# Optimization experiments

Measured on AMD Instinct MI355X. Metric: run time of the kernel, lower is better.

## Reference

```python
import jax, jax.numpy as jnp
import numpy as np


def setup_inputs() -> dict:
    key = jax.random.key(0)
    k1, k2 = jax.random.split(key)
    N = 4_194_304
    n, m = 63, 64
    x = jax.random.uniform(k1, (N,), dtype=jnp.float32)
    coefficients = jax.random.normal(k2, (n + 1 + m,), dtype=jnp.float32)
    return {"x": x, "coefficients": coefficients, "n": n, "m": m}


def reference(x, coefficients, n, m):
    # Split coefficients: numerator uses powers x^0..x^n, denominator x^1..x^m.
    n_coeffs = coefficients[: n + 1]
    m_coeffs = coefficients[n + 1 :]
    # x_powers_num: (n+1, N); tiny vector-matmul reduces power axis.
    exps_num = jnp.arange(n + 1, dtype=x.dtype)[:, None]
    numerator = jnp.einsum("p,pn->n", n_coeffs, x[None, :] ** exps_num)
    exps_den = jnp.arange(1, m + 1, dtype=x.dtype)[:, None]
    denominator = jnp.einsum("p,pn->n", m_coeffs, x[None, :] ** exps_den)
    return numerator / (jnp.abs(denominator) + 1.0)
```

## Files before the change

kernel.cpp:

```cpp
#include <hip/hip_runtime.h>


typedef float v2f __attribute__((ext_vector_type(2)));

#define EPT 8

__global__ __launch_bounds__(256) void rationals_kernel(
    const float* __restrict__ x,
    const float* __restrict__ coeff,
    float* __restrict__ out, int N) {
    int idx = (blockIdx.x * blockDim.x + threadIdx.x) * EPT;
    if (idx >= N) return;

    float xs[EPT];
    float4 xa = *reinterpret_cast<const float4*>(x + idx);
    float4 xb = *reinterpret_cast<const float4*>(x + idx + 4);
    xs[0] = xa.x; xs[1] = xa.y; xs[2] = xa.z; xs[3] = xa.w;
    xs[4] = xb.x; xs[5] = xb.y; xs[6] = xb.z; xs[7] = xb.w;

    v2f xx[EPT], h[EPT];
    float cn_top = coeff[63];
    float cd_top = coeff[127];
#pragma unroll
    for (int j = 0; j < EPT; ++j) {
        xx[j] = (v2f){xs[j], xs[j]};
        h[j]  = (v2f){cn_top, cd_top};
    }

#pragma unroll
    for (int p = 62; p >= 0; --p) {
        v2f c2 = {coeff[p], coeff[64 + p]};
#pragma unroll
        for (int j = 0; j < EPT; ++j)
            h[j] = __builtin_elementwise_fma(h[j], xx[j], c2);
    }

    float o[EPT];
#pragma unroll
    for (int j = 0; j < EPT; ++j) {
        float den = h[j].y * xs[j];
        o[j] = h[j].x * __builtin_amdgcn_rcpf(fabsf(den) + 1.0f);
    }
    *reinterpret_cast<float4*>(out + idx)     = (float4){o[0], o[1], o[2], o[3]};
    *reinterpret_cast<float4*>(out + idx + 4) = (float4){o[4], o[5], o[6], o[7]};
}

extern "C" void kernel_launch(void* const* d_in, const int* in_sizes, int n_in,
                              void* d_out, int out_size, void* d_ws, size_t ws_size,
                              hipStream_t stream) {
    const float* x     = (const float*)d_in[0];
    const float* coeff = (const float*)d_in[1];
    float* out = (float*)d_out;
    int N = in_sizes[0];

    int threads = 256;
    int elems_per_block = threads * EPT;
    int blocks = (N + elems_per_block - 1) / elems_per_block;
    rationals_kernel<<<blocks, threads, 0, stream>>>(x, coeff, out, N);
}
```

Before: 16.96 us.

## Split packed num/den Horner into separate scalar loops with 16 elements per thread

Replaces the paired v2f FMA, which evaluated numerator and denominator together, with two separate scalar Horner loops. Elements per thread rise from 8 to 16 to add independent FMA chains. This risks losing packed-FMA throughput unless the compiler re-packs adjacent elements, and it raises register pressure.

```diff
diff --git a/kernel.cpp b/kernel.cpp
--- a/kernel.cpp
+++ b/kernel.cpp
@@ -1,9 +1,7 @@
 #include <hip/hip_runtime.h>
 
 
-typedef float v2f __attribute__((ext_vector_type(2)));
-
-#define EPT 8
+#define EPT 16
 
 __global__ __launch_bounds__(256) void rationals_kernel(
     const float* __restrict__ x,
@@ -13,36 +11,50 @@
     if (idx >= N) return;
 
     float xs[EPT];
-    float4 xa = *reinterpret_cast<const float4*>(x + idx);
-    float4 xb = *reinterpret_cast<const float4*>(x + idx + 4);
-    xs[0] = xa.x; xs[1] = xa.y; xs[2] = xa.z; xs[3] = xa.w;
-    xs[4] = xb.x; xs[5] = xb.y; xs[6] = xb.z; xs[7] = xb.w;
-
-    v2f xx[EPT], h[EPT];
-    float cn_top = coeff[63];
-    float cd_top = coeff[127];
 #pragma unroll
-    for (int j = 0; j < EPT; ++j) {
-        xx[j] = (v2f){xs[j], xs[j]};
-        h[j]  = (v2f){cn_top, cd_top};
+    for (int j = 0; j < EPT; j += 4) {
+        float4 v = *reinterpret_cast<const float4*>(x + idx + j);
+        xs[j] = v.x; xs[j + 1] = v.y; xs[j + 2] = v.z; xs[j + 3] = v.w;
     }
 
+    float num[EPT];
+    {
+        float c = coeff[63];
 #pragma unroll
-    for (int p = 62; p >= 0; --p) {
-        v2f c2 = {coeff[p], coeff[64 + p]};
+        for (int j = 0; j < EPT; ++j) num[j] = c;
 #pragma unroll
-        for (int j = 0; j < EPT; ++j)
-            h[j] = __builtin_elementwise_fma(h[j], xx[j], c2);
+        for (int p = 62; p >= 0; --p) {
+            c = coeff[p];
+#pragma unroll
+            for (int j = 0; j < EPT; ++j)
+                num[j] = fmaf(num[j], xs[j], c);
+        }
+    }
+
+    float den[EPT];
+    {
+        float c = coeff[127];
+#pragma unroll
+        for (int j = 0; j < EPT; ++j) den[j] = c;
+#pragma unroll
+        for (int p = 126; p >= 64; --p) {
+            c = coeff[p];
+#pragma unroll
+            for (int j = 0; j < EPT; ++j)
+                den[j] = fmaf(den[j], xs[j], c);
+        }
     }
 
     float o[EPT];
 #pragma unroll
     for (int j = 0; j < EPT; ++j) {
-        float den = h[j].y * xs[j];
-        o[j] = h[j].x * __builtin_amdgcn_rcpf(fabsf(den) + 1.0f);
+        float d = den[j] * xs[j];
+        o[j] = num[j] * __builtin_amdgcn_rcpf(fabsf(d) + 1.0f);
     }
-    *reinterpret_cast<float4*>(out + idx)     = (float4){o[0], o[1], o[2], o[3]};
-    *reinterpret_cast<float4*>(out + idx + 4) = (float4){o[4], o[5], o[6], o[7]};
+#pragma unroll
+    for (int j = 0; j < EPT; j += 4)
+        *reinterpret_cast<float4*>(out + idx + j) =
+            (float4){o[j], o[j + 1], o[j + 2], o[j + 3]};
 }
 
 extern "C" void kernel_launch(void* const* d_in, const int* in_sizes, int n_in,
```

After: 20.44 us. +20.5%, slower.
